# Optimization experiments

Hardware: AMD Instinct MI355X
Metric: run time of the kernel (lower is better)

## Reference

```python
import jax, jax.numpy as jnp
import numpy as np

B, S, D, H = 2, 2048, 1024, 16
HD = D // H
EPS = 1e-5


def setup_inputs() -> dict:
    key = jax.random.key(0)
    ks = jax.random.split(key, 10)
    s = 1.0 / np.sqrt(D)
    return {
        "x": jax.random.normal(ks[0], (B, S, D), jnp.float32),
        "wq": jax.random.normal(ks[1], (D, D), jnp.float32) * s,
        "bq": jnp.zeros((D,), jnp.float32),
        "wk": jax.random.normal(ks[2], (D, D), jnp.float32) * s,
        "bk": jnp.zeros((D,), jnp.float32),
        "wv": jax.random.normal(ks[3], (D, D), jnp.float32) * s,
        "bv": jnp.zeros((D,), jnp.float32),
        "wo": jax.random.normal(ks[4], (D, D), jnp.float32) * s,
        "bo": jnp.zeros((D,), jnp.float32),
        "gamma": jnp.ones((D,), jnp.float32),
        "beta": jnp.zeros((D,), jnp.float32),
    }


def reference(x, wq, bq, wk, bk, wv, bv, wo, bo, gamma, beta):
    b, s, d = x.shape
    # QKV projections (torch Linear: y = x @ W^T + b)
    q = (x @ wq.T + bq).reshape(b, s, H, HD)
    k = (x @ wk.T + bk).reshape(b, s, H, HD)
    v = (x @ wv.T + bv).reshape(b, s, H, HD)
    # scores: [b, h, s, s], scaled by sqrt(d_model) as in the source
    scores = jnp.einsum("bqhd,bkhd->bhqk", q, k) / np.sqrt(D)
    attn = jax.nn.softmax(scores, axis=-1)
    ctx = jnp.einsum("bhqk,bkhd->bqhd", attn, v).reshape(b, s, d)
    # output projection (dropout is identity in eval mode)
    residual = ctx @ wo.T + bo
    y = x + residual
    # LayerNorm over last dim
    mu = jnp.mean(y, axis=-1, keepdims=True)
    var = jnp.var(y, axis=-1, keepdims=True)
    return (y - mu) / jnp.sqrt(var + EPS) * gamma + beta
```

## Files before the change

kernel.cpp:

```cpp
#include <hip/hip_runtime.h>
#include <math.h>

#define SS 2048
#define DMODEL 1024
#define NH 16
#define HD 64
#define MM 4096
#define LNEPS 1e-5f
#define CEXP 0.045084220029831766f

typedef __bf16 bf16_t;
typedef __bf16 bf16x4 __attribute__((ext_vector_type(4)));
typedef __bf16 bf16x8 __attribute__((ext_vector_type(8)));
typedef float f32x4 __attribute__((ext_vector_type(4)));
typedef float f32x16 __attribute__((ext_vector_type(16)));
typedef unsigned int u32;
typedef u32 u32x4 __attribute__((ext_vector_type(4)));

#define MFMA16(a, b, c) __builtin_amdgcn_mfma_f32_16x16x32_bf16(a, b, c, 0, 0, 0)
#define MFMA32(a, b, c) __builtin_amdgcn_mfma_f32_32x32x16_bf16(a, b, c, 0, 0, 0)

__device__ __forceinline__ void load_lds16(const bf16_t* g, bf16_t* l) {
    __builtin_amdgcn_global_load_lds(
        (const __attribute__((address_space(1))) void*)g,
        (__attribute__((address_space(3))) void*)l, 16, 0, 0);
}

__device__ __forceinline__ float fast_exp2(float x) {
#if __has_builtin(__builtin_amdgcn_exp2f)
    return __builtin_amdgcn_exp2f(x);
#else
    return exp2f(x);
#endif
}

__device__ __forceinline__ u32 pk2t(float lo, float hi) {
#if __has_builtin(__builtin_amdgcn_perm)
    return __builtin_amdgcn_perm(__float_as_uint(hi), __float_as_uint(lo),
                                 0x07060302u);
#else
    return (__float_as_uint(lo) >> 16) | (__float_as_uint(hi) & 0xFFFF0000u);
#endif
}

__global__ __launch_bounds__(256) void cvt_all(
    const float* __restrict__ x, const float* __restrict__ wq,
    const float* __restrict__ wk, const float* __restrict__ wv,
    const float* __restrict__ wo, bf16_t* __restrict__ out)
{
    int blk = blockIdx.x;
    const float* in;
    size_t off;
    if (blk < 4096)      { in = x;  off = 0; }
    else if (blk < 5120) { in = wq; off = 4194304; blk -= 4096; }
    else if (blk < 6144) { in = wk; off = 5242880; blk -= 5120; }
    else if (blk < 7168) { in = wv; off = 6291456; blk -= 6144; }
    else                 { in = wo; off = 7340032; blk -= 7168; }
    const int i = blk * 1024 + threadIdx.x * 4;
    float4 f = *(const float4*)(in + i);
    bf16x4 o = {(bf16_t)f.x, (bf16_t)f.y, (bf16_t)f.z, (bf16_t)f.w};
    *(bf16x4*)(out + off + i) = o;
}

__global__ __launch_bounds__(256, 2) void gemm_qkv(
    const bf16_t* __restrict__ A,
    const bf16_t* __restrict__ Wq, const bf16_t* __restrict__ Wk,
    const bf16_t* __restrict__ Wv,
    const float* __restrict__ bq, const float* __restrict__ bk,
    const float* __restrict__ bv,
    bf16_t* __restrict__ qo, bf16_t* __restrict__ ko, bf16_t* __restrict__ vo)
{
    __shared__ bf16_t As[128 * 32];
    __shared__ bf16_t Bs[128 * 32];
    const int tid = threadIdx.x, L = tid & 63, w = tid >> 6;
    const int quad = L >> 4, l15 = L & 15;
    const int wm = (w >> 1) * 64, wn = (w & 1) * 64;
    const int m0 = blockIdx.x * 128;
    const int mat = blockIdx.y >> 3;
    const int n0 = (blockIdx.y & 7) * 128;
    const bf16_t* W = (mat == 0) ? Wq : ((mat == 1) ? Wk : Wv);

    f32x4 acc[4][4] = {};
    for (int k0 = 0; k0 < DMODEL; k0 += 32) {
        __syncthreads();
        #pragma unroll
        for (int i = 0; i < 2; ++i) {
            const int r = w * 32 + i * 16;
            load_lds16(A + (size_t)(m0 + r + (L >> 2)) * DMODEL + k0 + (L & 3) * 8, &As[r * 32]);
            load_lds16(W + (size_t)(n0 + r + (L >> 2)) * DMODEL + k0 + (L & 3) * 8, &Bs[r * 32]);
        }
        __syncthreads();
        bf16x8 af[4], bfr[4];
        #pragma unroll
        for (int t = 0; t < 4; ++t) af[t] = *(const bf16x8*)&As[(wm + t * 16 + l15) * 32 + quad * 8];
        #pragma unroll
        for (int t = 0; t < 4; ++t) bfr[t] = *(const bf16x8*)&Bs[(wn + t * 16 + l15) * 32 + quad * 8];
        #pragma unroll
        for (int mt = 0; mt < 4; ++mt)
            #pragma unroll
            for (int nt = 0; nt < 4; ++nt)
                acc[mt][nt] = MFMA16(af[mt], bfr[nt], acc[mt][nt]);
    }

    if (mat < 2) {
        bf16_t* out = (mat == 0) ? qo : ko;
        const float* bias = (mat == 0) ? bq : bk;
        const float sc = (mat == 0) ? CEXP : 1.0f;
        #pragma unroll
        for (int nt = 0; nt < 4; ++nt) {
            const int gn = n0 + wn + nt * 16 + l15;
            const int h = gn >> 6, hd = gn & 63;
            const float bb = bias[gn];
            #pragma unroll
            for (int mt = 0; mt < 4; ++mt)
                #pragma unroll
                for (int r = 0; r < 4; ++r) {
                    const int gm = m0 + wm + mt * 16 + quad * 4 + r;
                    const int b = gm >> 11, s = gm & 2047;
                    out[((size_t)((b * NH + h) * SS + s)) * HD + hd] =
                        (bf16_t)((acc[mt][nt][r] + bb) * sc);
                }
        }
    } else {
        #pragma unroll
        for (int nt = 0; nt < 4; ++nt) {
            const int gn = n0 + wn + nt * 16 + l15;
            const int h = gn >> 6, hd = gn & 63;
            const float bb = bv[gn];
            #pragma unroll
            for (int mt = 0; mt < 4; ++mt) {
                const int gm0 = m0 + wm + mt * 16 + quad * 4;
                const int b = gm0 >> 11, s0 = gm0 & 2047;
                bf16x4 o = {(bf16_t)(acc[mt][nt][0] + bb), (bf16_t)(acc[mt][nt][1] + bb),
                            (bf16_t)(acc[mt][nt][2] + bb), (bf16_t)(acc[mt][nt][3] + bb)};
                *(bf16x4*)(vo + ((size_t)((b * NH + h) * HD + hd)) * SS + s0) = o;
            }
        }
    }
}

__global__ __launch_bounds__(256, 2) void gemm_out(
    const bf16_t* __restrict__ A, const bf16_t* __restrict__ W,
    const float* __restrict__ bias, const float* __restrict__ resid,
    float* __restrict__ out)
{
    __shared__ bf16_t As[128 * 32];
    __shared__ bf16_t Bs[128 * 32];
    const int tid = threadIdx.x, L = tid & 63, w = tid >> 6;
    const int quad = L >> 4, l15 = L & 15;
    const int wm = (w >> 1) * 64, wn = (w & 1) * 64;
    const int m0 = blockIdx.x * 128;
    const int n0 = blockIdx.y * 128;

    f32x4 acc[4][4] = {};
    for (int k0 = 0; k0 < DMODEL; k0 += 32) {
        __syncthreads();
        #pragma unroll
        for (int i = 0; i < 2; ++i) {
            const int r = w * 32 + i * 16;
            load_lds16(A + (size_t)(m0 + r + (L >> 2)) * DMODEL + k0 + (L & 3) * 8, &As[r * 32]);
            load_lds16(W + (size_t)(n0 + r + (L >> 2)) * DMODEL + k0 + (L & 3) * 8, &Bs[r * 32]);
        }
        __syncthreads();
        bf16x8 af[4], bfr[4];
        #pragma unroll
        for (int t = 0; t < 4; ++t) af[t] = *(const bf16x8*)&As[(wm + t * 16 + l15) * 32 + quad * 8];
        #pragma unroll
        for (int t = 0; t < 4; ++t) bfr[t] = *(const bf16x8*)&Bs[(wn + t * 16 + l15) * 32 + quad * 8];
        #pragma unroll
        for (int mt = 0; mt < 4; ++mt)
            #pragma unroll
            for (int nt = 0; nt < 4; ++nt)
                acc[mt][nt] = MFMA16(af[mt], bfr[nt], acc[mt][nt]);
    }
    #pragma unroll
    for (int nt = 0; nt < 4; ++nt) {
        const int gn = n0 + wn + nt * 16 + l15;
        const float bb = bias[gn];
        #pragma unroll
        for (int mt = 0; mt < 4; ++mt)
            #pragma unroll
            for (int r = 0; r < 4; ++r) {
                const int gm = m0 + wm + mt * 16 + quad * 4 + r;
                const size_t idx = (size_t)gm * DMODEL + gn;
                out[idx] = acc[mt][nt][r] + bb + resid[idx];
            }
    }
}

__global__ __launch_bounds__(256, 2) void flash_kernel(
    const bf16_t* __restrict__ Q, const bf16_t* __restrict__ K,
    const bf16_t* __restrict__ VT, bf16_t* __restrict__ ctx)
{
    __shared__ bf16_t Kt[128 * 64];
    __shared__ bf16_t Vt[64 * 128];
    const int tid = threadIdx.x, L = tid & 63, w = tid >> 6;
    const int ql = L & 31, hh = L >> 5;
    const int bh = blockIdx.y, b = bh >> 4, h = bh & 15;
    const int q0 = blockIdx.x * 128;
    const bf16_t* Qb = Q + (size_t)bh * SS * HD;
    const bf16_t* Kb = K + (size_t)bh * SS * HD;
    const bf16_t* Vb = VT + (size_t)bh * HD * SS;

    const int qrow = q0 + w * 32 + ql;
    bf16x8 qf[4];
    #pragma unroll
    for (int c = 0; c < 4; ++c)
        qf[c] = *(const bf16x8*)(Qb + (size_t)qrow * HD + c * 16 + hh * 8);

    f32x16 accO[2] = {};
    float l_s = 0.f;

    const int srow = L >> 3;
    const int kchk = ((L & 7) ^ srow) * 8;
    const int vsub = L >> 4;

    for (int kt = 0; kt < 16; ++kt) {
        const int kb = kt * 128;
        __syncthreads();
        #pragma unroll
        for (int i = 0; i < 4; ++i) {
            const int r0 = w * 32 + i * 8;
            load_lds16(Kb + (size_t)(kb + r0 + srow) * HD + kchk, &Kt[r0 * 64]);
        }
        #pragma unroll
        for (int i = 0; i < 4; ++i) {
            const int r0 = w * 16 + i * 4;
            const int vr = r0 + vsub;
            load_lds16(Vb + (size_t)vr * SS + kb + ((L & 15) ^ (vr & 15)) * 8, &Vt[r0 * 128]);
        }
        __syncthreads();

        #pragma unroll
        for (int g = 0; g < 4; ++g) {
            const int krow = (g * 32 + ql) * 64;
            f32x16 st = {};
            #pragma unroll
            for (int mf = 0; mf < 4; ++mf) {
                bf16x8 kf = *(const bf16x8*)&Kt[krow + (((mf * 2 + hh) ^ (L & 7)) * 8)];
                st = MFMA32(kf, qf[mf], st);
            }
            float p[16];
            #pragma unroll
            for (int r = 0; r < 16; ++r) p[r] = fast_exp2(st[r]);
            float t0 = ((p[0] + p[1]) + (p[2] + p[3])) + ((p[4] + p[5]) + (p[6] + p[7]));
            float t1 = ((p[8] + p[9]) + (p[10] + p[11])) + ((p[12] + p[13]) + (p[14] + p[15]));
            l_s += t0 + t1;

            u32x4 pu0 = {pk2t(p[0], p[1]), pk2t(p[2], p[3]),
                         pk2t(p[4], p[5]), pk2t(p[6], p[7])};
            u32x4 pu1 = {pk2t(p[8], p[9]), pk2t(p[10], p[11]),
                         pk2t(p[12], p[13]), pk2t(p[14], p[15])};
            bf16x8 pb0 = __builtin_bit_cast(bf16x8, pu0);
            bf16x8 pb1 = __builtin_bit_cast(bf16x8, pu1);

            #pragma unroll
            for (int tile = 0; tile < 2; ++tile) {
                const int vbase = (tile * 32 + ql) * 128;
                const int sw = ql & 15;
                #pragma unroll
                for (int p8 = 0; p8 < 2; ++p8) {
                    const int lc0 = g * 4 + 2 * p8;
                    bf16x4 lo = *(const bf16x4*)&Vt[vbase + ((lc0 ^ sw) * 8) + 4 * hh];
                    bf16x4 hi = *(const bf16x4*)&Vt[vbase + (((lc0 + 1) ^ sw) * 8) + 4 * hh];
                    bf16x8 va = __builtin_shufflevector(lo, hi, 0, 1, 2, 3, 4, 5, 6, 7);
                    accO[tile] = MFMA32(va, (p8 == 0) ? pb0 : pb1, accO[tile]);
                }
            }
        }
    }

    l_s += __shfl_xor(l_s, 32);
    const float inv = 1.0f / l_s;
    bf16_t* crow = ctx + ((size_t)(b * SS + qrow)) * DMODEL + h * HD;
    #pragma unroll
    for (int tile = 0; tile < 2; ++tile)
        #pragma unroll
        for (int a = 0; a < 4; ++a) {
            const int r = 4 * a;
            bf16x4 o = {(bf16_t)(accO[tile][r] * inv), (bf16_t)(accO[tile][r + 1] * inv),
                        (bf16_t)(accO[tile][r + 2] * inv), (bf16_t)(accO[tile][r + 3] * inv)};
            *(bf16x4*)(crow + tile * 32 + 8 * a + 4 * hh) = o;
        }
}

__global__ __launch_bounds__(256) void layernorm_kernel(
    float* __restrict__ y, const float* __restrict__ gamma,
    const float* __restrict__ beta)
{
    const int row = blockIdx.x;
    const int tid = threadIdx.x;
    float* yr = y + (size_t)row * DMODEL;
    float4 v = ((const float4*)yr)[tid];
    float s = v.x + v.y + v.z + v.w;
    float ss = v.x * v.x + v.y * v.y + v.z * v.z + v.w * v.w;
    #pragma unroll
    for (int off = 32; off >= 1; off >>= 1) {
        s += __shfl_xor(s, off);
        ss += __shfl_xor(ss, off);
    }
    __shared__ float red[8];
    const int wid = tid >> 6, lane = tid & 63;
    if (lane == 0) { red[wid] = s; red[4 + wid] = ss; }
    __syncthreads();
    s = red[0] + red[1] + red[2] + red[3];
    ss = red[4] + red[5] + red[6] + red[7];
    const float mu = s * (1.0f / DMODEL);
    const float var = ss * (1.0f / DMODEL) - mu * mu;
    const float inv = rsqrtf(var + LNEPS);
    float4 g = ((const float4*)gamma)[tid];
    float4 be = ((const float4*)beta)[tid];
    float4 o;
    o.x = (v.x - mu) * inv * g.x + be.x;
    o.y = (v.y - mu) * inv * g.y + be.y;
    o.z = (v.z - mu) * inv * g.z + be.z;
    o.w = (v.w - mu) * inv * g.w + be.w;
    ((float4*)yr)[tid] = o;
}

extern "C" void kernel_launch(void* const* d_in, const int* in_sizes, int n_in,
                              void* d_out, int out_size, void* d_ws, size_t ws_size,
                              hipStream_t stream)
{
    const float* x     = (const float*)d_in[0];
    const float* wq    = (const float*)d_in[1];
    const float* bq    = (const float*)d_in[2];
    const float* wk    = (const float*)d_in[3];
    const float* bk    = (const float*)d_in[4];
    const float* wv    = (const float*)d_in[5];
    const float* bv    = (const float*)d_in[6];
    const float* wo    = (const float*)d_in[7];
    const float* bo    = (const float*)d_in[8];
    const float* gamma = (const float*)d_in[9];
    const float* beta  = (const float*)d_in[10];
    float* out = (float*)d_out;

    bf16_t* xb  = (bf16_t*)d_ws;
    bf16_t* wqb = xb + (size_t)4194304;
    bf16_t* wkb = wqb + (size_t)1048576;
    bf16_t* wvb = wkb + (size_t)1048576;
    bf16_t* wob = wvb + (size_t)1048576;
    bf16_t* qb  = xb + (size_t)8388608;
    bf16_t* kb  = qb + (size_t)4194304;
    bf16_t* vtb = kb + (size_t)4194304;
    bf16_t* ctx = vtb + (size_t)4194304;

    cvt_all<<<8192, 256, 0, stream>>>(x, wq, wk, wv, wo, xb);
    gemm_qkv<<<dim3(32, 24), 256, 0, stream>>>(xb, wqb, wkb, wvb, bq, bk, bv, qb, kb, vtb);
    flash_kernel<<<dim3(16, 32), 256, 0, stream>>>(qb, kb, vtb, ctx);
    gemm_out<<<dim3(32, 8), 256, 0, stream>>>(ctx, wob, bo, x, out);
    layernorm_kernel<<<MM, 256, 0, stream>>>(out, gamma, beta);
}
```

Baseline: 209.7 us.

## Split flash key range across two wave groups and deepen GEMM K-tile with swizzle

The flash kernel now launches 512 threads per block. Two groups of four waves each process alternating halves of the key tiles, then reduce their partial outputs and row sums through LDS before writing the context. This doubles the waves per query block to hide latency, at the cost of an extra reduction and more LDS. Separately, both GEMMs move from a 32-wide to a 64-wide K step with an XOR-swizzled LDS layout, which halves the barriers per K and aims to avoid bank conflicts. The softmax has no max subtraction, so splitting the key range is safe as plain sums.

New measurement: 237.2 us. 1.13x slower.

```diff
diff --git a/kernel.cpp b/kernel.cpp
--- a/kernel.cpp
+++ b/kernel.cpp
@@ -70,8 +70,8 @@
     const float* __restrict__ bv,
     bf16_t* __restrict__ qo, bf16_t* __restrict__ ko, bf16_t* __restrict__ vo)
 {
-    __shared__ bf16_t As[128 * 32];
-    __shared__ bf16_t Bs[128 * 32];
+    __shared__ bf16_t As[128 * 64];
+    __shared__ bf16_t Bs[128 * 64];
     const int tid = threadIdx.x, L = tid & 63, w = tid >> 6;
     const int quad = L >> 4, l15 = L & 15;
     const int wm = (w >> 1) * 64, wn = (w & 1) * 64;
@@ -79,27 +79,35 @@
     const int mat = blockIdx.y >> 3;
     const int n0 = (blockIdx.y & 7) * 128;
     const bf16_t* W = (mat == 0) ? Wq : ((mat == 1) ? Wk : Wv);
+    const int schk = ((L & 7) ^ (L >> 3)) * 8;
 
     f32x4 acc[4][4] = {};
-    for (int k0 = 0; k0 < DMODEL; k0 += 32) {
-        __syncthreads();
-        #pragma unroll
-        for (int i = 0; i < 2; ++i) {
-            const int r = w * 32 + i * 16;
-            load_lds16(A + (size_t)(m0 + r + (L >> 2)) * DMODEL + k0 + (L & 3) * 8, &As[r * 32]);
-            load_lds16(W + (size_t)(n0 + r + (L >> 2)) * DMODEL + k0 + (L & 3) * 8, &Bs[r * 32]);
-        }
-        __syncthreads();
-        bf16x8 af[4], bfr[4];
-        #pragma unroll
-        for (int t = 0; t < 4; ++t) af[t] = *(const bf16x8*)&As[(wm + t * 16 + l15) * 32 + quad * 8];
-        #pragma unroll
-        for (int t = 0; t < 4; ++t) bfr[t] = *(const bf16x8*)&Bs[(wn + t * 16 + l15) * 32 + quad * 8];
-        #pragma unroll
-        for (int mt = 0; mt < 4; ++mt)
-            #pragma unroll
-            for (int nt = 0; nt < 4; ++nt)
-                acc[mt][nt] = MFMA16(af[mt], bfr[nt], acc[mt][nt]);
+    for (int k0 = 0; k0 < DMODEL; k0 += 64) {
+        __syncthreads();
+        #pragma unroll
+        for (int i = 0; i < 4; ++i) {
+            const int r = w * 32 + i * 8;
+            load_lds16(A + (size_t)(m0 + r + (L >> 3)) * DMODEL + k0 + schk, &As[r * 64]);
+            load_lds16(W + (size_t)(n0 + r + (L >> 3)) * DMODEL + k0 + schk, &Bs[r * 64]);
+        }
+        __syncthreads();
+        #pragma unroll
+        for (int c = 0; c < 2; ++c) {
+            bf16x8 af[4], bfr[4];
+            #pragma unroll
+            for (int t = 0; t < 4; ++t)
+                af[t] = *(const bf16x8*)&As[(wm + t * 16 + l15) * 64 +
+                                            (((c * 4 + quad) ^ (l15 & 7)) * 8)];
+            #pragma unroll
+            for (int t = 0; t < 4; ++t)
+                bfr[t] = *(const bf16x8*)&Bs[(wn + t * 16 + l15) * 64 +
+                                             (((c * 4 + quad) ^ (l15 & 7)) * 8)];
+            #pragma unroll
+            for (int mt = 0; mt < 4; ++mt)
+                #pragma unroll
+                for (int nt = 0; nt < 4; ++nt)
+                    acc[mt][nt] = MFMA16(af[mt], bfr[nt], acc[mt][nt]);
+        }
     }
 
     if (mat < 2) {
@@ -144,34 +152,42 @@
     const float* __restrict__ bias, const float* __restrict__ resid,
     float* __restrict__ out)
 {
-    __shared__ bf16_t As[128 * 32];
-    __shared__ bf16_t Bs[128 * 32];
+    __shared__ bf16_t As[128 * 64];
+    __shared__ bf16_t Bs[128 * 64];
     const int tid = threadIdx.x, L = tid & 63, w = tid >> 6;
     const int quad = L >> 4, l15 = L & 15;
     const int wm = (w >> 1) * 64, wn = (w & 1) * 64;
     const int m0 = blockIdx.x * 128;
     const int n0 = blockIdx.y * 128;
+    const int schk = ((L & 7) ^ (L >> 3)) * 8;
 
     f32x4 acc[4][4] = {};
-    for (int k0 = 0; k0 < DMODEL; k0 += 32) {
-        __syncthreads();
-        #pragma unroll
-        for (int i = 0; i < 2; ++i) {
-            const int r = w * 32 + i * 16;
-            load_lds16(A + (size_t)(m0 + r + (L >> 2)) * DMODEL + k0 + (L & 3) * 8, &As[r * 32]);
-            load_lds16(W + (size_t)(n0 + r + (L >> 2)) * DMODEL + k0 + (L & 3) * 8, &Bs[r * 32]);
-        }
-        __syncthreads();
-        bf16x8 af[4], bfr[4];
-        #pragma unroll
-        for (int t = 0; t < 4; ++t) af[t] = *(const bf16x8*)&As[(wm + t * 16 + l15) * 32 + quad * 8];
-        #pragma unroll
-        for (int t = 0; t < 4; ++t) bfr[t] = *(const bf16x8*)&Bs[(wn + t * 16 + l15) * 32 + quad * 8];
-        #pragma unroll
-        for (int mt = 0; mt < 4; ++mt)
-            #pragma unroll
-            for (int nt = 0; nt < 4; ++nt)
-                acc[mt][nt] = MFMA16(af[mt], bfr[nt], acc[mt][nt]);
+    for (int k0 = 0; k0 < DMODEL; k0 += 64) {
+        __syncthreads();
+        #pragma unroll
+        for (int i = 0; i < 4; ++i) {
+            const int r = w * 32 + i * 8;
+            load_lds16(A + (size_t)(m0 + r + (L >> 3)) * DMODEL + k0 + schk, &As[r * 64]);
+            load_lds16(W + (size_t)(n0 + r + (L >> 3)) * DMODEL + k0 + schk, &Bs[r * 64]);
+        }
+        __syncthreads();
+        #pragma unroll
+        for (int c = 0; c < 2; ++c) {
+            bf16x8 af[4], bfr[4];
+            #pragma unroll
+            for (int t = 0; t < 4; ++t)
+                af[t] = *(const bf16x8*)&As[(wm + t * 16 + l15) * 64 +
+                                            (((c * 4 + quad) ^ (l15 & 7)) * 8)];
+            #pragma unroll
+            for (int t = 0; t < 4; ++t)
+                bfr[t] = *(const bf16x8*)&Bs[(wn + t * 16 + l15) * 64 +
+                                             (((c * 4 + quad) ^ (l15 & 7)) * 8)];
+            #pragma unroll
+            for (int mt = 0; mt < 4; ++mt)
+                #pragma unroll
+                for (int nt = 0; nt < 4; ++nt)
+                    acc[mt][nt] = MFMA16(af[mt], bfr[nt], acc[mt][nt]);
+        }
     }
     #pragma unroll
     for (int nt = 0; nt < 4; ++nt) {
@@ -188,21 +204,23 @@
     }
 }
 
-__global__ __launch_bounds__(256, 2) void flash_kernel(
+__global__ __launch_bounds__(512, 4) void flash_kernel(
     const bf16_t* __restrict__ Q, const bf16_t* __restrict__ K,
     const bf16_t* __restrict__ VT, bf16_t* __restrict__ ctx)
 {
-    __shared__ bf16_t Kt[128 * 64];
-    __shared__ bf16_t Vt[64 * 128];
-    const int tid = threadIdx.x, L = tid & 63, w = tid >> 6;
+    __shared__ bf16_t smem[32768];
+    const int tid = threadIdx.x, L = tid & 63;
+    const int w8 = tid >> 6, grp = w8 >> 2, wq = w8 & 3;
     const int ql = L & 31, hh = L >> 5;
     const int bh = blockIdx.y, b = bh >> 4, h = bh & 15;
     const int q0 = blockIdx.x * 128;
     const bf16_t* Qb = Q + (size_t)bh * SS * HD;
     const bf16_t* Kb = K + (size_t)bh * SS * HD;
     const bf16_t* Vb = VT + (size_t)bh * HD * SS;
-
-    const int qrow = q0 + w * 32 + ql;
+    bf16_t* Kt = smem + grp * 16384;
+    bf16_t* Vt = Kt + 8192;
+
+    const int qrow = q0 + wq * 32 + ql;
     bf16x8 qf[4];
     #pragma unroll
     for (int c = 0; c < 4; ++c)
@@ -215,17 +233,17 @@
     const int kchk = ((L & 7) ^ srow) * 8;
     const int vsub = L >> 4;
 
-    for (int kt = 0; kt < 16; ++kt) {
-        const int kb = kt * 128;
+    for (int p = 0; p < 8; ++p) {
+        const int kb = (2 * p + grp) * 128;
         __syncthreads();
         #pragma unroll
         for (int i = 0; i < 4; ++i) {
-            const int r0 = w * 32 + i * 8;
+            const int r0 = wq * 32 + i * 8;
             load_lds16(Kb + (size_t)(kb + r0 + srow) * HD + kchk, &Kt[r0 * 64]);
         }
         #pragma unroll
         for (int i = 0; i < 4; ++i) {
-            const int r0 = w * 16 + i * 4;
+            const int r0 = wq * 16 + i * 4;
             const int vr = r0 + vsub;
             load_lds16(Vb + (size_t)vr * SS + kb + ((L & 15) ^ (vr & 15)) * 8, &Vt[r0 * 128]);
         }
@@ -240,17 +258,17 @@
                 bf16x8 kf = *(const bf16x8*)&Kt[krow + (((mf * 2 + hh) ^ (L & 7)) * 8)];
                 st = MFMA32(kf, qf[mf], st);
             }
-            float p[16];
-            #pragma unroll
-            for (int r = 0; r < 16; ++r) p[r] = fast_exp2(st[r]);
-            float t0 = ((p[0] + p[1]) + (p[2] + p[3])) + ((p[4] + p[5]) + (p[6] + p[7]));
-            float t1 = ((p[8] + p[9]) + (p[10] + p[11])) + ((p[12] + p[13]) + (p[14] + p[15]));
+            float pv[16];
+            #pragma unroll
+            for (int r = 0; r < 16; ++r) pv[r] = fast_exp2(st[r]);
+            float t0 = ((pv[0] + pv[1]) + (pv[2] + pv[3])) + ((pv[4] + pv[5]) + (pv[6] + pv[7]));
+            float t1 = ((pv[8] + pv[9]) + (pv[10] + pv[11])) + ((pv[12] + pv[13]) + (pv[14] + pv[15]));
             l_s += t0 + t1;
 
-            u32x4 pu0 = {pk2t(p[0], p[1]), pk2t(p[2], p[3]),
-                         pk2t(p[4], p[5]), pk2t(p[6], p[7])};
-            u32x4 pu1 = {pk2t(p[8], p[9]), pk2t(p[10], p[11]),
-                         pk2t(p[12], p[13]), pk2t(p[14], p[15])};
+            u32x4 pu0 = {pk2t(pv[0], pv[1]), pk2t(pv[2], pv[3]),
+                         pk2t(pv[4], pv[5]), pk2t(pv[6], pv[7])};
+            u32x4 pu1 = {pk2t(pv[8], pv[9]), pk2t(pv[10], pv[11]),
+                         pk2t(pv[12], pv[13]), pk2t(pv[14], pv[15])};
             bf16x8 pb0 = __builtin_bit_cast(bf16x8, pu0);
             bf16x8 pb1 = __builtin_bit_cast(bf16x8, pu1);
 
@@ -270,18 +288,38 @@
         }
     }
 
-    l_s += __shfl_xor(l_s, 32);
-    const float inv = 1.0f / l_s;
-    bf16_t* crow = ctx + ((size_t)(b * SS + qrow)) * DMODEL + h * HD;
-    #pragma unroll
-    for (int tile = 0; tile < 2; ++tile)
-        #pragma unroll
-        for (int a = 0; a < 4; ++a) {
-            const int r = 4 * a;
-            bf16x4 o = {(bf16_t)(accO[tile][r] * inv), (bf16_t)(accO[tile][r + 1] * inv),
-                        (bf16_t)(accO[tile][r + 2] * inv), (bf16_t)(accO[tile][r + 3] * inv)};
-            *(bf16x4*)(crow + tile * 32 + 8 * a + 4 * hh) = o;
-        }
+    __syncthreads();
+    float* cb = (float*)smem;
+    const int cbase = (wq * 64 + L) * 33;
+    if (grp == 1) {
+        #pragma unroll
+        for (int tile = 0; tile < 2; ++tile)
+            #pragma unroll
+            for (int r = 0; r < 16; ++r)
+                cb[cbase + tile * 16 + r] = accO[tile][r];
+        cb[cbase + 32] = l_s;
+    }
+    __syncthreads();
+    if (grp == 0) {
+        #pragma unroll
+        for (int tile = 0; tile < 2; ++tile)
+            #pragma unroll
+            for (int r = 0; r < 16; ++r)
+                accO[tile][r] += cb[cbase + tile * 16 + r];
+        l_s += cb[cbase + 32];
+        l_s += __shfl_xor(l_s, 32);
+        const float inv = 1.0f / l_s;
+        bf16_t* crow = ctx + ((size_t)(b * SS + qrow)) * DMODEL + h * HD;
+        #pragma unroll
+        for (int tile = 0; tile < 2; ++tile)
+            #pragma unroll
+            for (int a = 0; a < 4; ++a) {
+                const int r = 4 * a;
+                bf16x4 o = {(bf16_t)(accO[tile][r] * inv), (bf16_t)(accO[tile][r + 1] * inv),
+                            (bf16_t)(accO[tile][r + 2] * inv), (bf16_t)(accO[tile][r + 3] * inv)};
+                *(bf16x4*)(crow + tile * 32 + 8 * a + 4 * hh) = o;
+            }
+    }
 }
 
 __global__ __launch_bounds__(256) void layernorm_kernel(
@@ -347,7 +385,7 @@
 
     cvt_all<<<8192, 256, 0, stream>>>(x, wq, wk, wv, wo, xb);
     gemm_qkv<<<dim3(32, 24), 256, 0, stream>>>(xb, wqb, wkb, wvb, bq, bk, bv, qb, kb, vtb);
-    flash_kernel<<<dim3(16, 32), 256, 0, stream>>>(qb, kb, vtb, ctx);
+    flash_kernel<<<dim3(16, 32), 512, 0, stream>>>(qb, kb, vtb, ctx);
     gemm_out<<<dim3(32, 8), 256, 0, stream>>>(ctx, wob, bo, x, out);
     layernorm_kernel<<<MM, 256, 0, stream>>>(out, gamma, beta);
 }
```

## Double-buffer K/V LDS tiles in flash attention kernel

Applied to the files above, without the earlier changes.

Splits the flash attention inner loop into a load stage and a compute stage, and ping-pongs between two LDS buffer sets for K and V. The async global-to-LDS loads for the next tile are issued before computing on the current tile, so memory latency can overlap with the MFMA and exp work instead of sitting behind a barrier. This doubles per-block LDS to 64KB, which may pressure occupancy at two blocks per CU. It also relies on the compiler's waitcnt placement not serialising the loads.

Result: no change. 212.5 us (+1.3%).

```diff
diff --git a/kernel.cpp b/kernel.cpp
--- a/kernel.cpp
+++ b/kernel.cpp
@@ -188,12 +188,76 @@
     }
 }
 
+__device__ __forceinline__ void flash_stage(
+    bf16_t (&Kt)[8192], bf16_t (&Vt)[8192],
+    const bf16_t* __restrict__ Kb, const bf16_t* __restrict__ Vb, int kb,
+    int w, int L, int srow, int kchk, int vsub)
+{
+    #pragma unroll
+    for (int i = 0; i < 4; ++i) {
+        const int r0 = w * 32 + i * 8;
+        load_lds16(Kb + (size_t)(kb + r0 + srow) * HD + kchk, &Kt[r0 * 64]);
+    }
+    #pragma unroll
+    for (int i = 0; i < 4; ++i) {
+        const int r0 = w * 16 + i * 4;
+        const int vr = r0 + vsub;
+        load_lds16(Vb + (size_t)vr * SS + kb + ((L & 15) ^ (vr & 15)) * 8, &Vt[r0 * 128]);
+    }
+}
+
+__device__ __forceinline__ void flash_compute(
+    const bf16_t (&Kt)[8192], const bf16_t (&Vt)[8192],
+    const bf16x8 (&qf)[4], f32x16 (&accO)[2], float& l_s,
+    int ql, int hh, int L)
+{
+    #pragma unroll
+    for (int g = 0; g < 4; ++g) {
+        const int krow = (g * 32 + ql) * 64;
+        f32x16 st = {};
+        #pragma unroll
+        for (int mf = 0; mf < 4; ++mf) {
+            bf16x8 kf = *(const bf16x8*)&Kt[krow + (((mf * 2 + hh) ^ (L & 7)) * 8)];
+            st = MFMA32(kf, qf[mf], st);
+        }
+        float pv[16];
+        #pragma unroll
+        for (int r = 0; r < 16; ++r) pv[r] = fast_exp2(st[r]);
+        float t0 = ((pv[0] + pv[1]) + (pv[2] + pv[3])) + ((pv[4] + pv[5]) + (pv[6] + pv[7]));
+        float t1 = ((pv[8] + pv[9]) + (pv[10] + pv[11])) + ((pv[12] + pv[13]) + (pv[14] + pv[15]));
+        l_s += t0 + t1;
+
+        u32x4 pu0 = {pk2t(pv[0], pv[1]), pk2t(pv[2], pv[3]),
+                     pk2t(pv[4], pv[5]), pk2t(pv[6], pv[7])};
+        u32x4 pu1 = {pk2t(pv[8], pv[9]), pk2t(pv[10], pv[11]),
+                     pk2t(pv[12], pv[13]), pk2t(pv[14], pv[15])};
+        bf16x8 pb0 = __builtin_bit_cast(bf16x8, pu0);
+        bf16x8 pb1 = __builtin_bit_cast(bf16x8, pu1);
+
+        #pragma unroll
+        for (int tile = 0; tile < 2; ++tile) {
+            const int vbase = (tile * 32 + ql) * 128;
+            const int sw = ql & 15;
+            #pragma unroll
+            for (int p8 = 0; p8 < 2; ++p8) {
+                const int lc0 = g * 4 + 2 * p8;
+                bf16x4 lo = *(const bf16x4*)&Vt[vbase + ((lc0 ^ sw) * 8) + 4 * hh];
+                bf16x4 hi = *(const bf16x4*)&Vt[vbase + (((lc0 + 1) ^ sw) * 8) + 4 * hh];
+                bf16x8 va = __builtin_shufflevector(lo, hi, 0, 1, 2, 3, 4, 5, 6, 7);
+                accO[tile] = MFMA32(va, (p8 == 0) ? pb0 : pb1, accO[tile]);
+            }
+        }
+    }
+}
+
 __global__ __launch_bounds__(256, 2) void flash_kernel(
     const bf16_t* __restrict__ Q, const bf16_t* __restrict__ K,
     const bf16_t* __restrict__ VT, bf16_t* __restrict__ ctx)
 {
-    __shared__ bf16_t Kt[128 * 64];
-    __shared__ bf16_t Vt[64 * 128];
+    __shared__ bf16_t KtA[8192];
+    __shared__ bf16_t VtA[8192];
+    __shared__ bf16_t KtB[8192];
+    __shared__ bf16_t VtB[8192];
     const int tid = threadIdx.x, L = tid & 63, w = tid >> 6;
     const int ql = L & 31, hh = L >> 5;
     const int bh = blockIdx.y, b = bh >> 4, h = bh & 15;
@@ -215,59 +279,16 @@
     const int kchk = ((L & 7) ^ srow) * 8;
     const int vsub = L >> 4;
 
-    for (int kt = 0; kt < 16; ++kt) {
-        const int kb = kt * 128;
-        __syncthreads();
-        #pragma unroll
-        for (int i = 0; i < 4; ++i) {
-            const int r0 = w * 32 + i * 8;
-            load_lds16(Kb + (size_t)(kb + r0 + srow) * HD + kchk, &Kt[r0 * 64]);
-        }
-        #pragma unroll
-        for (int i = 0; i < 4; ++i) {
-            const int r0 = w * 16 + i * 4;
-            const int vr = r0 + vsub;
-            load_lds16(Vb + (size_t)vr * SS + kb + ((L & 15) ^ (vr & 15)) * 8, &Vt[r0 * 128]);
-        }
-        __syncthreads();
-
-        #pragma unroll
-        for (int g = 0; g < 4; ++g) {
-            const int krow = (g * 32 + ql) * 64;
-            f32x16 st = {};
-            #pragma unroll
-            for (int mf = 0; mf < 4; ++mf) {
-                bf16x8 kf = *(const bf16x8*)&Kt[krow + (((mf * 2 + hh) ^ (L & 7)) * 8)];
-                st = MFMA32(kf, qf[mf], st);
-            }
-            float p[16];
-            #pragma unroll
-            for (int r = 0; r < 16; ++r) p[r] = fast_exp2(st[r]);
-            float t0 = ((p[0] + p[1]) + (p[2] + p[3])) + ((p[4] + p[5]) + (p[6] + p[7]));
-            float t1 = ((p[8] + p[9]) + (p[10] + p[11])) + ((p[12] + p[13]) + (p[14] + p[15]));
-            l_s += t0 + t1;
-
-            u32x4 pu0 = {pk2t(p[0], p[1]), pk2t(p[2], p[3]),
-                         pk2t(p[4], p[5]), pk2t(p[6], p[7])};
-            u32x4 pu1 = {pk2t(p[8], p[9]), pk2t(p[10], p[11]),
-                         pk2t(p[12], p[13]), pk2t(p[14], p[15])};
-            bf16x8 pb0 = __builtin_bit_cast(bf16x8, pu0);
-            bf16x8 pb1 = __builtin_bit_cast(bf16x8, pu1);
-
-            #pragma unroll
-            for (int tile = 0; tile < 2; ++tile) {
-                const int vbase = (tile * 32 + ql) * 128;
-                const int sw = ql & 15;
-                #pragma unroll
-                for (int p8 = 0; p8 < 2; ++p8) {
-                    const int lc0 = g * 4 + 2 * p8;
-                    bf16x4 lo = *(const bf16x4*)&Vt[vbase + ((lc0 ^ sw) * 8) + 4 * hh];
-                    bf16x4 hi = *(const bf16x4*)&Vt[vbase + (((lc0 + 1) ^ sw) * 8) + 4 * hh];
-                    bf16x8 va = __builtin_shufflevector(lo, hi, 0, 1, 2, 3, 4, 5, 6, 7);
-                    accO[tile] = MFMA32(va, (p8 == 0) ? pb0 : pb1, accO[tile]);
-                }
-            }
-        }
+    flash_stage(KtA, VtA, Kb, Vb, 0, w, L, srow, kchk, vsub);
+    #pragma unroll 1
+    for (int kt2 = 0; kt2 < 8; ++kt2) {
+        __syncthreads();
+        flash_stage(KtB, VtB, Kb, Vb, (2 * kt2 + 1) * 128, w, L, srow, kchk, vsub);
+        flash_compute(KtA, VtA, qf, accO, l_s, ql, hh, L);
+        __syncthreads();
+        if (kt2 < 7)
+            flash_stage(KtA, VtA, Kb, Vb, (2 * kt2 + 2) * 128, w, L, srow, kchk, vsub);
+        flash_compute(KtB, VtB, qf, accO, l_s, ql, hh, L);
     }
 
     l_s += __shfl_xor(l_s, 32);
```
